# Kernel tuning notes

Hardware: AMD Instinct MI355X
Metric: run time of the kernel (lower is better)

The kernel has to match this reference:

```python
import jax, jax.numpy as jnp
import numpy as np

B, T, D = 4, 4096, 2048
W_SCALE = 0.02


def setup_inputs() -> dict:
    key = jax.random.key(0)
    ks = jax.random.split(key, 10)
    x = jax.random.normal(ks[0], (B, T, D), dtype=jnp.float32)
    Wk = jax.random.normal(ks[1], (D, D), dtype=jnp.float32) * W_SCALE
    Wv = jax.random.normal(ks[2], (D, D), dtype=jnp.float32) * W_SCALE
    Wr = jax.random.normal(ks[3], (D, D), dtype=jnp.float32) * W_SCALE
    Wo = jax.random.normal(ks[4], (D, D), dtype=jnp.float32) * W_SCALE
    bk = jnp.zeros((D,), jnp.float32)
    bv = jnp.zeros((D,), jnp.float32)
    br = jnp.zeros((D,), jnp.float32)
    bo = jnp.zeros((D,), jnp.float32)
    tmk = jax.random.uniform(ks[5], (D,), dtype=jnp.float32)
    tmv = jax.random.uniform(ks[6], (D,), dtype=jnp.float32)
    tmr = jax.random.uniform(ks[7], (D,), dtype=jnp.float32)
    u = jax.random.normal(ks[8], (D,), dtype=jnp.float32) * 0.1
    w = jax.random.uniform(ks[9], (D,), dtype=jnp.float32)  # positive decay
    return {"x": x, "Wk": Wk, "bk": bk, "Wv": Wv, "bv": bv, "Wr": Wr, "br": br,
            "Wo": Wo, "bo": bo, "tmk": tmk, "tmv": tmv, "tmr": tmr, "u": u, "w": w}


def reference(x, Wk, bk, Wv, bv, Wr, br, Wo, bo, tmk, tmv, tmr, u, w):
    # time-shift: xs[:, t] = x[:, t-1], xs[:, 0] = 0  (ZeroPad2d((0,0,1,-1)))
    xs = jnp.pad(x, ((0, 0), (1, 0), (0, 0)))[:, :-1]
    k = x * tmk + xs * (1.0 - tmk)
    v = x * tmv + xs * (1.0 - tmv)
    r = jax.nn.silu(x * tmr + xs * (1.0 - tmr))
    # torch nn.Linear: y = x @ W.T + b
    k = jnp.einsum('btd,ed->bte', k, Wk) + bk
    v = jnp.einsum('btd,ed->bte', v, Wv) + bv
    r = jnp.einsum('btd,ed->bte', r, Wr) + br

    def step(carry, kv_t):
        a, b = carry  # (B, D) each
        k_t, v_t = kv_t
        t = jnp.maximum(u + k_t, w)
        e1 = jnp.exp(-w - t)
        e2 = jnp.exp(u + k_t - t)
        a = e1 * a + e2 * v_t
        b = e1 * b + e2
        return (a, b), a / b

    a0 = jnp.zeros((x.shape[0], x.shape[2]), x.dtype)
    b0 = jnp.zeros_like(a0)
    # scan over time: (T, B, D)
    _, wkv = jax.lax.scan(step, (a0, b0), (k.transpose(1, 0, 2), v.transpose(1, 0, 2)))
    wkv = wkv.transpose(1, 0, 2)  # (B, T, D)
    return jnp.einsum('btd,ed->bte', wkv * r, Wo) + bo
```

## Files before the change

kernel.cpp:

```cpp
#include <hip/hip_runtime.h>
#include <hip/hip_bf16.h>

#define Bb 4
#define Tt 4096
#define Dd 2048
#define Mm (Bb*Tt)
#define CHUNK 64
#define NCHUNK (Tt/CHUNK)

typedef short  short8  __attribute__((ext_vector_type(8)));
typedef float  floatx4 __attribute__((ext_vector_type(4)));

static __device__ __forceinline__ short f2bf(float f) {
    union { float f; unsigned u; } x; x.f = f;
    unsigned r = x.u + 0x7fffu + ((x.u >> 16) & 1u);
    return (short)(r >> 16);
}
static __device__ __forceinline__ float bf2f(short s) {
    union { unsigned u; float f; } x; x.u = ((unsigned)(unsigned short)s) << 16;
    return x.f;
}
static __device__ __forceinline__ float siluf(float v) { return v / (1.f + __expf(-v)); }
static __device__ __forceinline__ float mixf(float xv, float sv, float tv) {
    return fmaf(tv, xv - sv, sv);
}

#define GLDS16(gp, lp) __builtin_amdgcn_global_load_lds( \
    (const __attribute__((address_space(1))) void*)(gp), \
    (__attribute__((address_space(3))) void*)(lp), 16, 0, 0)

static __device__ __forceinline__ short8 pack8(float4 a, float4 b) {
    short8 r;
    r[0]=f2bf(a.x); r[1]=f2bf(a.y); r[2]=f2bf(a.z); r[3]=f2bf(a.w);
    r[4]=f2bf(b.x); r[5]=f2bf(b.y); r[6]=f2bf(b.z); r[7]=f2bf(b.w);
    return r;
}

__global__ __launch_bounds__(256)
void prep_w(const float* __restrict__ w0, const float* __restrict__ w1,
            const float* __restrict__ w2, const float* __restrict__ w3,
            short* __restrict__ o0, short* __restrict__ o1,
            short* __restrict__ o2, short* __restrict__ o3)
{
    const float* s; short* d;
    switch (blockIdx.y) {
        case 0: s = w0; d = o0; break;
        case 1: s = w1; d = o1; break;
        case 2: s = w2; d = o2; break;
        default: s = w3; d = o3; break;
    }
    const size_t e = ((size_t)blockIdx.x * 256 + threadIdx.x) * 8;
    float4 a = *(const float4*)(s + e);
    float4 b = *(const float4*)(s + e + 4);
    *(short8*)(d + e) = pack8(a, b);
}

__global__ __launch_bounds__(256)
void prep_a(const float* __restrict__ x,
            const float* __restrict__ tmk, const float* __restrict__ tmv,
            const float* __restrict__ tmr,
            short* __restrict__ ka, short* __restrict__ va, short* __restrict__ ra)
{
    const size_t e = ((size_t)blockIdx.x * 256 + threadIdx.x) * 8;
    const size_t row = e >> 11;
    const int    col = (int)(e & (Dd - 1));
    const int    t   = (int)(row & (Tt - 1));

    const float* xp = x + e;
    float4 x0 = *(const float4*)xp, x1 = *(const float4*)(xp + 4);
    float4 s0 = make_float4(0,0,0,0), s1 = make_float4(0,0,0,0);
    if (t > 0) { s0 = *(const float4*)(xp - Dd); s1 = *(const float4*)(xp - Dd + 4); }

    float4 tk0 = *(const float4*)(tmk + col), tk1 = *(const float4*)(tmk + col + 4);
    float4 tv0 = *(const float4*)(tmv + col), tv1 = *(const float4*)(tmv + col + 4);
    float4 tr0 = *(const float4*)(tmr + col), tr1 = *(const float4*)(tmr + col + 4);

    float4 k0 = make_float4(mixf(x0.x,s0.x,tk0.x), mixf(x0.y,s0.y,tk0.y),
                            mixf(x0.z,s0.z,tk0.z), mixf(x0.w,s0.w,tk0.w));
    float4 k1 = make_float4(mixf(x1.x,s1.x,tk1.x), mixf(x1.y,s1.y,tk1.y),
                            mixf(x1.z,s1.z,tk1.z), mixf(x1.w,s1.w,tk1.w));
    float4 v0 = make_float4(mixf(x0.x,s0.x,tv0.x), mixf(x0.y,s0.y,tv0.y),
                            mixf(x0.z,s0.z,tv0.z), mixf(x0.w,s0.w,tv0.w));
    float4 v1 = make_float4(mixf(x1.x,s1.x,tv1.x), mixf(x1.y,s1.y,tv1.y),
                            mixf(x1.z,s1.z,tv1.z), mixf(x1.w,s1.w,tv1.w));
    float4 r0 = make_float4(siluf(mixf(x0.x,s0.x,tr0.x)), siluf(mixf(x0.y,s0.y,tr0.y)),
                            siluf(mixf(x0.z,s0.z,tr0.z)), siluf(mixf(x0.w,s0.w,tr0.w)));
    float4 r1 = make_float4(siluf(mixf(x1.x,s1.x,tr1.x)), siluf(mixf(x1.y,s1.y,tr1.y)),
                            siluf(mixf(x1.z,s1.z,tr1.z)), siluf(mixf(x1.w,s1.w,tr1.w)));

    *(short8*)(ka + e) = pack8(k0, k1);
    *(short8*)(va + e) = pack8(v0, v1);
    *(short8*)(ra + e) = pack8(r0, r1);
}

template<int OUTBF>
__global__ __launch_bounds__(256)
void gemm_bf16(const short* __restrict__ A, const short* __restrict__ B,
               const float* __restrict__ bias, void* __restrict__ Cout)
{
    __shared__ short As[128*32];
    __shared__ short Bs[128*32];

    const int tid  = threadIdx.x;
    const int lane = tid & 63, wave = tid >> 6;
    const int row0 = blockIdx.x * 128;
    const int col0 = blockIdx.y * 128;

    const int srow = wave * 32 + (lane >> 2);
    const int scol = (lane & 3) * 8;
    const short* Ag0 = A + (size_t)(row0 + srow) * Dd + scol;
    const short* Ag1 = Ag0 + (size_t)16 * Dd;
    const short* Bg0 = B + (size_t)(col0 + srow) * Dd + scol;
    const short* Bg1 = Bg0 + (size_t)16 * Dd;
    short* Al0 = As + (wave * 32     ) * 32;
    short* Al1 = As + (wave * 32 + 16) * 32;
    short* Bl0 = Bs + (wave * 32     ) * 32;
    short* Bl1 = Bs + (wave * 32 + 16) * 32;

    const int wm = (wave >> 1) * 64, wn = (wave & 1) * 64;
    const int fm = lane & 15, fq = lane >> 4;

    floatx4 acc[4][4];
    #pragma unroll
    for (int i = 0; i < 4; i++)
        #pragma unroll
        for (int j = 0; j < 4; j++) acc[i][j] = (floatx4){0.f,0.f,0.f,0.f};

    for (int k0 = 0; k0 < Dd; k0 += 32) {
        __syncthreads();
        GLDS16(Ag0, Al0);
        GLDS16(Ag1, Al1);
        GLDS16(Bg0, Bl0);
        GLDS16(Bg1, Bl1);
        Ag0 += 32; Ag1 += 32; Bg0 += 32; Bg1 += 32;
        __syncthreads();

        short8 af[4], bfv[4];
        #pragma unroll
        for (int i = 0; i < 4; i++)
            af[i] = *(const short8*)(As + (wm + i*16 + fm)*32 + fq*8);
        #pragma unroll
        for (int j = 0; j < 4; j++)
            bfv[j] = *(const short8*)(Bs + (wn + j*16 + fm)*32 + fq*8);
        #pragma unroll
        for (int i = 0; i < 4; i++)
            #pragma unroll
            for (int j = 0; j < 4; j++)
                acc[i][j] = __builtin_amdgcn_mfma_f32_16x16x32_bf16(af[i], bfv[j], acc[i][j], 0, 0, 0);
    }

    #pragma unroll
    for (int j = 0; j < 4; j++) {
        const int gc = col0 + wn + j*16 + fm;
        const float bj = bias[gc];
        #pragma unroll
        for (int i = 0; i < 4; i++) {
            const int gr = row0 + wm + i*16 + fq*4;
            #pragma unroll
            for (int r = 0; r < 4; r++) {
                const float v = acc[i][j][r] + bj;
                if constexpr (OUTBF)
                    ((short*)Cout)[(size_t)(gr + r) * Dd + gc] = f2bf(v);
                else
                    ((float*)Cout)[(size_t)(gr + r) * Dd + gc] = v;
            }
        }
    }
}

__global__ __launch_bounds__(256)
void scan1(const short* __restrict__ K, const short* __restrict__ V,
           const float* __restrict__ u, const float* __restrict__ w,
           float* __restrict__ Asum, float* __restrict__ Bsum, float* __restrict__ Dsum)
{
    const int c = blockIdx.x, b = blockIdx.y;
    const int d = blockIdx.z * 256 + threadIdx.x;
    const float uu = u[d], ww = w[d];
    const size_t base = ((size_t)(b*Tt + c*CHUNK)) * Dd + d;
    float a = 0.f, bb = 0.f, dd = 1.f;
    #pragma unroll 4
    for (int t = 0; t < CHUNK; t++) {
        const float k = bf2f(K[base + (size_t)t*Dd]);
        const float v = bf2f(V[base + (size_t)t*Dd]);
        const float tt = fmaxf(uu + k, ww);
        const float e1 = __expf(-ww - tt);
        const float e2 = __expf(uu + k - tt);
        a  = e1*a  + e2*v;
        bb = e1*bb + e2;
        dd *= e1;
    }
    const size_t idx = ((size_t)c*Bb + b) * Dd + d;
    Asum[idx] = a; Bsum[idx] = bb; Dsum[idx] = dd;
}

__global__ __launch_bounds__(256)
void scan2(const float* __restrict__ Asum, const float* __restrict__ Bsum,
           const float* __restrict__ Dsum, float* __restrict__ Sa, float* __restrict__ Sb)
{
    const int g = blockIdx.x * 256 + threadIdx.x;
    float a = 0.f, bb = 0.f;
    for (int c = 0; c < NCHUNK; c++) {
        const size_t idx = (size_t)c * (Bb*Dd) + g;
        Sa[idx] = a; Sb[idx] = bb;
        const float dd = Dsum[idx];
        a  = dd*a  + Asum[idx];
        bb = dd*bb + Bsum[idx];
    }
}

__global__ __launch_bounds__(256)
void scan3(const short* __restrict__ K, const short* __restrict__ V,
           const short* __restrict__ R,
           const float* __restrict__ Sa, const float* __restrict__ Sb,
           const float* __restrict__ u, const float* __restrict__ w,
           short* __restrict__ AF)
{
    const int c = blockIdx.x, b = blockIdx.y;
    const int d = blockIdx.z * 256 + threadIdx.x;
    const float uu = u[d], ww = w[d];
    const size_t sidx = ((size_t)c*Bb + b) * Dd + d;
    float a = Sa[sidx], bb = Sb[sidx];
    const size_t base = ((size_t)(b*Tt + c*CHUNK)) * Dd + d;
    #pragma unroll 4
    for (int t = 0; t < CHUNK; t++) {
        const float k = bf2f(K[base + (size_t)t*Dd]);
        const float v = bf2f(V[base + (size_t)t*Dd]);
        const float tt = fmaxf(uu + k, ww);
        const float e1 = __expf(-ww - tt);
        const float e2 = __expf(uu + k - tt);
        a  = e1*a  + e2*v;
        bb = e1*bb + e2;
        const float wkv = a / bb;
        const float r = bf2f(R[base + (size_t)t*Dd]);
        AF[base + (size_t)t*Dd] = f2bf(wkv * r);
    }
}

extern "C" void kernel_launch(void* const* d_in, const int* in_sizes, int n_in,
                              void* d_out, int out_size, void* d_ws, size_t ws_size,
                              hipStream_t stream)
{
    const float* x   = (const float*)d_in[0];
    const float* Wk  = (const float*)d_in[1];
    const float* bk  = (const float*)d_in[2];
    const float* Wv  = (const float*)d_in[3];
    const float* bv  = (const float*)d_in[4];
    const float* Wr  = (const float*)d_in[5];
    const float* br  = (const float*)d_in[6];
    const float* Wo  = (const float*)d_in[7];
    const float* bo  = (const float*)d_in[8];
    const float* tmk = (const float*)d_in[9];
    const float* tmv = (const float*)d_in[10];
    const float* tmr = (const float*)d_in[11];
    const float* u   = (const float*)d_in[12];
    const float* w   = (const float*)d_in[13];

    char* ws = (char*)d_ws;
    short* Wkb  = (short*)(ws + 0x00000000ull);
    short* Wvb  = (short*)(ws + 0x00800000ull);
    short* Wrb  = (short*)(ws + 0x01000000ull);
    short* Wob  = (short*)(ws + 0x01800000ull);
    short* ka   = (short*)(ws + 0x02000000ull);
    short* va   = (short*)(ws + 0x06000000ull);
    short* ra   = (short*)(ws + 0x0A000000ull);
    short* Kb   = (short*)(ws + 0x0E000000ull);
    short* Vb   = (short*)(ws + 0x12000000ull);
    short* Rb   = (short*)(ws + 0x16000000ull);
    float* Asum = (float*)(ws + 0x1A000000ull);
    float* Bsum = (float*)(ws + 0x1A200000ull);
    float* Dsum = (float*)(ws + 0x1A400000ull);
    float* Sa   = (float*)(ws + 0x1A600000ull);
    float* Sb   = (float*)(ws + 0x1A800000ull);
    short* AF   = ka;

    prep_w<<<dim3(2048, 4), 256, 0, stream>>>(Wk, Wv, Wr, Wo, Wkb, Wvb, Wrb, Wob);
    prep_a<<<dim3(16384), 256, 0, stream>>>(x, tmk, tmv, tmr, ka, va, ra);

    dim3 gg(Mm/128, Dd/128);
    gemm_bf16<1><<<gg, 256, 0, stream>>>(ka, Wkb, bk, Kb);
    gemm_bf16<1><<<gg, 256, 0, stream>>>(va, Wvb, bv, Vb);
    gemm_bf16<1><<<gg, 256, 0, stream>>>(ra, Wrb, br, Rb);

    scan1<<<dim3(NCHUNK, Bb, Dd/256), 256, 0, stream>>>(Kb, Vb, u, w, Asum, Bsum, Dsum);
    scan2<<<dim3((Bb*Dd)/256), 256, 0, stream>>>(Asum, Bsum, Dsum, Sa, Sb);
    scan3<<<dim3(NCHUNK, Bb, Dd/256), 256, 0, stream>>>(Kb, Vb, Rb, Sa, Sb, u, w, AF);

    gemm_bf16<0><<<gg, 256, 0, stream>>>(AF, Wob, bo, (float*)d_out);
}
```

Before: 1.141 ms.

## Double-buffer A tile, load B directly to registers, stage bf16 epilogue via LDS

The GEMM now double-buffers the A tile in shared memory and prefetches the next K-slice while computing the current one, which removes one barrier per iteration. B fragments are loaded straight from global memory into registers instead of going through LDS. The bf16 output is staged through LDS so each row is written with coalesced 16-byte stores. The trade-offs are higher register pressure and uncoalesced per-lane global reads for B.

```diff
diff --git a/kernel.cpp b/kernel.cpp
--- a/kernel.cpp
+++ b/kernel.cpp
@@ -98,8 +98,7 @@
 void gemm_bf16(const short* __restrict__ A, const short* __restrict__ B,
                const float* __restrict__ bias, void* __restrict__ Cout)
 {
-    __shared__ short As[128*32];
-    __shared__ short Bs[128*32];
+    __shared__ short As[2][128*32];
 
     const int tid  = threadIdx.x;
     const int lane = tid & 63, wave = tid >> 6;
@@ -110,15 +109,15 @@
     const int scol = (lane & 3) * 8;
     const short* Ag0 = A + (size_t)(row0 + srow) * Dd + scol;
     const short* Ag1 = Ag0 + (size_t)16 * Dd;
-    const short* Bg0 = B + (size_t)(col0 + srow) * Dd + scol;
-    const short* Bg1 = Bg0 + (size_t)16 * Dd;
-    short* Al0 = As + (wave * 32     ) * 32;
-    short* Al1 = As + (wave * 32 + 16) * 32;
-    short* Bl0 = Bs + (wave * 32     ) * 32;
-    short* Bl1 = Bs + (wave * 32 + 16) * 32;
+    const int wslot = wave * 32 * 32;
 
     const int wm = (wave >> 1) * 64, wn = (wave & 1) * 64;
     const int fm = lane & 15, fq = lane >> 4;
+
+    const short* Bg[4];
+    #pragma unroll
+    for (int j = 0; j < 4; j++)
+        Bg[j] = B + (size_t)(col0 + wn + j*16 + fm) * Dd + fq*8;
 
     floatx4 acc[4][4];
     #pragma unroll
@@ -126,43 +125,85 @@
         #pragma unroll
         for (int j = 0; j < 4; j++) acc[i][j] = (floatx4){0.f,0.f,0.f,0.f};
 
-    for (int k0 = 0; k0 < Dd; k0 += 32) {
+    GLDS16(Ag0, &As[0][wslot]);
+    GLDS16(Ag1, &As[0][wslot + 16*32]);
+    Ag0 += 32; Ag1 += 32;
+    short8 breg0[4], breg1[4];
+    #pragma unroll
+    for (int j = 0; j < 4; j++) { breg0[j] = *(const short8*)Bg[j]; Bg[j] += 32; }
+
+    short8 af[4];
+    #pragma unroll 1
+    for (int e = 0; e < Dd/32; e += 2) {
         __syncthreads();
-        GLDS16(Ag0, Al0);
-        GLDS16(Ag1, Al1);
-        GLDS16(Bg0, Bl0);
-        GLDS16(Bg1, Bl1);
-        Ag0 += 32; Ag1 += 32; Bg0 += 32; Bg1 += 32;
-        __syncthreads();
-
-        short8 af[4], bfv[4];
+        GLDS16(Ag0, &As[1][wslot]);
+        GLDS16(Ag1, &As[1][wslot + 16*32]);
+        Ag0 += 32; Ag1 += 32;
+        #pragma unroll
+        for (int j = 0; j < 4; j++) { breg1[j] = *(const short8*)Bg[j]; Bg[j] += 32; }
         #pragma unroll
         for (int i = 0; i < 4; i++)
-            af[i] = *(const short8*)(As + (wm + i*16 + fm)*32 + fq*8);
-        #pragma unroll
-        for (int j = 0; j < 4; j++)
-            bfv[j] = *(const short8*)(Bs + (wn + j*16 + fm)*32 + fq*8);
+            af[i] = *(const short8*)(&As[0][(wm + i*16 + fm)*32 + fq*8]);
         #pragma unroll
         for (int i = 0; i < 4; i++)
             #pragma unroll
             for (int j = 0; j < 4; j++)
-                acc[i][j] = __builtin_amdgcn_mfma_f32_16x16x32_bf16(af[i], bfv[j], acc[i][j], 0, 0, 0);
-    }
-
-    #pragma unroll
-    for (int j = 0; j < 4; j++) {
-        const int gc = col0 + wn + j*16 + fm;
-        const float bj = bias[gc];
-        #pragma unroll
-        for (int i = 0; i < 4; i++) {
-            const int gr = row0 + wm + i*16 + fq*4;
+                acc[i][j] = __builtin_amdgcn_mfma_f32_16x16x32_bf16(af[i], breg0[j], acc[i][j], 0, 0, 0);
+
+        __syncthreads();
+        GLDS16(Ag0, &As[0][wslot]);
+        GLDS16(Ag1, &As[0][wslot + 16*32]);
+        Ag0 += 32; Ag1 += 32;
+        #pragma unroll
+        for (int j = 0; j < 4; j++) { breg0[j] = *(const short8*)Bg[j]; Bg[j] += 32; }
+        #pragma unroll
+        for (int i = 0; i < 4; i++)
+            af[i] = *(const short8*)(&As[1][(wm + i*16 + fm)*32 + fq*8]);
+        #pragma unroll
+        for (int i = 0; i < 4; i++)
             #pragma unroll
-            for (int r = 0; r < 4; r++) {
-                const float v = acc[i][j][r] + bj;
-                if constexpr (OUTBF)
-                    ((short*)Cout)[(size_t)(gr + r) * Dd + gc] = f2bf(v);
-                else
-                    ((float*)Cout)[(size_t)(gr + r) * Dd + gc] = v;
+            for (int j = 0; j < 4; j++)
+                acc[i][j] = __builtin_amdgcn_mfma_f32_16x16x32_bf16(af[i], breg1[j], acc[i][j], 0, 0, 0);
+    }
+
+    if constexpr (OUTBF) {
+        short* SL = &As[0][0];
+        float bj[4];
+        #pragma unroll
+        for (int j = 0; j < 4; j++) bj[j] = bias[col0 + wn + j*16 + fm];
+        #pragma unroll 1
+        for (int h = 0; h < 2; ++h) {
+            __syncthreads();
+            if ((wave >> 1) == h) {
+                #pragma unroll
+                for (int i = 0; i < 4; i++)
+                    #pragma unroll
+                    for (int j = 0; j < 4; j++)
+                        #pragma unroll
+                        for (int r = 0; r < 4; r++)
+                            SL[(i*16 + fq*4 + r)*128 + wn + j*16 + fm] =
+                                f2bf(acc[i][j][r] + bj[j]);
+            }
+            __syncthreads();
+            #pragma unroll
+            for (int q = 0; q < 4; q++) {
+                const int lin = q*256 + tid;
+                const int r = lin >> 4, c = (lin & 15) * 8;
+                *(short8*)((short*)Cout + (size_t)(row0 + h*64 + r) * Dd + col0 + c)
+                    = *(const short8*)(SL + r*128 + c);
+            }
+        }
+    } else {
+        #pragma unroll
+        for (int j = 0; j < 4; j++) {
+            const int gc = col0 + wn + j*16 + fm;
+            const float bj = bias[gc];
+            #pragma unroll
+            for (int i = 0; i < 4; i++) {
+                const int gr = row0 + wm + i*16 + fq*4;
+                #pragma unroll
+                for (int r = 0; r < 4; r++)
+                    ((float*)Cout)[(size_t)(gr + r) * Dd + gc] = acc[i][j][r] + bj;
             }
         }
     }
```

Measured after the change: 1.714 ms. +50.2%, slower.
